# Optimization experiments

Hardware: AMD Instinct MI355X
Metric: run time of the kernel (lower is better)

The kernel has to match this reference:

```python
import jax, jax.numpy as jnp
import numpy as np

EPS = 1e-6     # vnn repo EPS used in VN nonlinearity / batchnorm norm
BN_EPS = 1e-5  # torch BatchNorm default eps
K = 40         # args.n_knn


def knn_idx(x, k):
    # x: (B, 3, N) -> (B, N, k) indices of k nearest neighbors (incl. self)
    inner = -2.0 * jnp.einsum('bdn,bdm->bnm', x, x)
    xx = jnp.sum(x * x, axis=1)  # (B, N)
    neg_dist = -xx[:, :, None] - inner - xx[:, None, :]
    _, idx = jax.lax.top_k(neg_dist, k)
    return idx


def get_graph_feature_cross(x, k):
    # x: (B, 3, N) -> (B, 3, 3, N, k): channels are [nbr - ctr, ctr, cross(nbr, ctr)]
    pts = jnp.transpose(x, (0, 2, 1))  # (B, N, 3)
    idx = knn_idx(x, k)                # (B, N, k)
    nbr = jax.vmap(lambda p, i: p[i])(pts, idx)          # (B, N, k, 3)
    ctr = jnp.broadcast_to(pts[:, :, None, :], nbr.shape)
    cross = jnp.cross(nbr, ctr)
    feat = jnp.stack([nbr - ctr, ctr, cross], axis=3)    # (B, N, k, 3, 3)
    return jnp.transpose(feat, (0, 3, 4, 1, 2))          # (B, C=3, 3vec, N, k)


def vn_bn(x):
    # VNBatchNorm (training-mode batch stats, affine = identity at init)
    # x: (B, C, 3, *rest); normalize the per-vector norm across (B, *rest)
    norm = jnp.sqrt(jnp.sum(x * x, axis=2)) + EPS  # (B, C, *rest)
    axes = (0,) + tuple(range(2, norm.ndim))
    mean = jnp.mean(norm, axis=axes, keepdims=True)
    var = jnp.var(norm, axis=axes, keepdims=True)
    norm_bn = (norm - mean) / jnp.sqrt(var + BN_EPS)
    return x / jnp.expand_dims(norm, 2) * jnp.expand_dims(norm_bn, 2)


def vn_lin(W, x):
    # channel-wise linear on axis 1 of (B, C, 3, ...)
    return jnp.einsum('oc,bc...->bo...', W, x)


def vn_lrelu(x, Wf, Wd):
    # VNLinearLeakyReLU with negative_slope=0.0
    p = vn_bn(vn_lin(Wf, x))
    d = vn_lin(Wd, x)
    dot = jnp.sum(p * d, axis=2, keepdims=True)
    dsq = jnp.sum(d * d, axis=2, keepdims=True)
    neg = p - (dot / (dsq + EPS)) * d  # project out the d component
    return jnp.where(dot >= 0, p, neg)


def vn_max_pool(x, W):
    # pool over last axis, picking the element maximizing <x, d> per (B, C, n)
    d = vn_lin(W, x)
    dot = jnp.sum(x * d, axis=2, keepdims=True)          # (B, C, 1, ..., K)
    idx = jnp.argmax(dot, axis=-1, keepdims=True)        # (B, C, 1, ..., 1)
    idx = jnp.broadcast_to(idx, x.shape[:-1] + (1,))
    return jnp.take_along_axis(x, idx, axis=-1)[..., 0]


def setup_inputs() -> dict:
    key = jax.random.key(0)
    ks = jax.random.split(key, 16)
    def w(k, o, i):
        bound = 1.0 / np.sqrt(i)  # torch nn.Linear default init
        return jax.random.uniform(k, (o, i), jnp.float32, -bound, bound)
    B, N = 8, 2048
    C1, C2, C3 = 64 // 3, 128 // 3, 1024 // 3  # 21, 42, 341
    F1, F2 = 512 // 3, 256 // 3                # 170, 85
    return {
        'x': jax.random.normal(ks[0], (B, 3, N), jnp.float32),
        'W_pos_feat': w(ks[1], C1, 3), 'W_pos_dir': w(ks[2], C1, 3),
        'W_gpool': w(ks[3], C1, C1),
        'W1_feat': w(ks[4], C1, C1), 'W1_dir': w(ks[5], C1, C1),
        'W2_feat': w(ks[6], C2, C1), 'W2_dir': w(ks[7], C2, C1),
        'W3_feat': w(ks[8], C3, C2), 'W3_dir': w(ks[9], C3, C2),
        'W_pool': w(ks[10], C3, C3),
        'Wf1_feat': w(ks[11], F1, C3), 'Wf1_dir': w(ks[12], F1, C3),
        'Wf2_feat': w(ks[13], F2, F1), 'Wf2_dir': w(ks[14], F2, F1),
        'Wf3': w(ks[15], 3, F2),
    }


def reference(x, W_pos_feat, W_pos_dir, W_gpool, W1_feat, W1_dir, W2_feat, W2_dir,
              W3_feat, W3_dir, W_pool, Wf1_feat, Wf1_dir, Wf2_feat, Wf2_dir, Wf3):
    feat = get_graph_feature_cross(x, K)            # (B, 3, 3, N, K)
    h = vn_lrelu(feat, W_pos_feat, W_pos_dir)       # (B, 21, 3, N, K)
    h = vn_max_pool(h, W_gpool)                     # (B, 21, 3, N)
    h = vn_lrelu(h, W1_feat, W1_dir)                # (B, 21, 3, N)
    h = vn_lrelu(h, W2_feat, W2_dir)                # (B, 42, 3, N)
    h = vn_lrelu(h, W3_feat, W3_dir)                # (B, 341, 3, N)
    h = vn_max_pool(h, W_pool)                      # (B, 341, 3)
    h = vn_lrelu(h, Wf1_feat, Wf1_dir)              # (B, 170, 3)
    h = vn_lrelu(h, Wf2_feat, Wf2_dir)              # (B, 85, 3)
    return vn_lin(Wf3, h)                           # (B, 3, 3)
```

## Files before the change

### kernel.cpp

```cpp
#include <hip/hip_runtime.h>

#define NP 2048
#define BATCH 8
#define KNN 40
#define EPSF 1e-6f
#define BNEPS 1e-5f

typedef __attribute__((ext_vector_type(8))) short short8;
typedef __attribute__((ext_vector_type(4))) float f32x4;

__device__ __forceinline__ unsigned ordf(float v){
  unsigned u = __float_as_uint(v);
  return (u & 0x80000000u) ? ~u : (u | 0x80000000u);
}

__device__ __forceinline__ void bsplit(float v, unsigned short &h, unsigned short &l){
  unsigned u = __float_as_uint(v);
  unsigned hu = (u + 0x7fffu + ((u >> 16) & 1u)) >> 16;
  h = (unsigned short)hu;
  float r = v - __uint_as_float(hu << 16);
  unsigned u2 = __float_as_uint(r);
  l = (unsigned short)((u2 + 0x7fffu + ((u2 >> 16) & 1u)) >> 16);
}

__device__ __forceinline__ float bf2f(unsigned short h){
  return __uint_as_float(((unsigned)h) << 16);
}

__global__ __launch_bounds__(256) void knn_kernel(const float* __restrict__ x, int* __restrict__ idx){
  __shared__ float4 sP[NP];
  int tid = threadIdx.x;
  int w = tid >> 6, lane = tid & 63;
  int row0 = blockIdx.x * 8 + w * 2, row1 = row0 + 1;
  int b = row0 >> 11;
  int i0 = row0 & 2047, i1 = row1 & 2047;
  const float* xb = x + b * 3 * NP;
  for (int t = tid; t < NP; t += 256){
    float a = xb[t], c = xb[NP + t], d = xb[2*NP + t];
    float xx = __fadd_rn(__fadd_rn(__fmul_rn(a,a), __fmul_rn(c,c)), __fmul_rn(d,d));
    sP[t] = make_float4(a, c, d, xx);
  }
  __syncthreads();
  float4 pa = sP[i0];
  float4 pb = sP[i1];
  const float4* lp = &sP[lane];
  unsigned long long a0 = 0, a1 = 0, a2 = 0, a3 = 0;
  unsigned long long b0 = 0, b1 = 0, b2 = 0, b3 = 0;
  #pragma unroll
  for (int m = 0; m < 32; m++){
    float4 pj = lp[m * 64];
    unsigned lowbits = (unsigned)(2047 - (m*64 + lane));
    float dotA = __fadd_rn(__fadd_rn(__fmul_rn(pa.x, pj.x), __fmul_rn(pa.y, pj.y)), __fmul_rn(pa.z, pj.z));
    float vA = __fsub_rn(__fsub_rn(-pa.w, __fmul_rn(-2.f, dotA)), pj.w);
    unsigned long long pkA = ((unsigned long long)ordf(vA) << 32) | lowbits;
    if (pkA > a3){
      if (pkA > a2){ a3 = a2; if (pkA > a1){ a2 = a1; if (pkA > a0){ a1 = a0; a0 = pkA; } else a1 = pkA; } else a2 = pkA; }
      else a3 = pkA;
    }
    float dotB = __fadd_rn(__fadd_rn(__fmul_rn(pb.x, pj.x), __fmul_rn(pb.y, pj.y)), __fmul_rn(pb.z, pj.z));
    float vB = __fsub_rn(__fsub_rn(-pb.w, __fmul_rn(-2.f, dotB)), pj.w);
    unsigned long long pkB = ((unsigned long long)ordf(vB) << 32) | lowbits;
    if (pkB > b3){
      if (pkB > b2){ b3 = b2; if (pkB > b1){ b2 = b1; if (pkB > b0){ b1 = b0; b0 = pkB; } else b1 = pkB; } else b2 = pkB; }
      else b3 = pkB;
    }
  }
  unsigned outA = 0, outB = 0;
  unsigned long long lastA = ~0ull, lastB = ~0ull;
  for (int kk = 0; kk < KNN; kk++){
    unsigned hvA = (unsigned)(a0 >> 32), hvB = (unsigned)(b0 >> 32);
    unsigned vmA = hvA, vmB = hvB;
    #pragma unroll
    for (int st = 32; st > 0; st >>= 1){
      unsigned oA = (unsigned)__shfl_xor((int)vmA, st, 64);
      unsigned oB = (unsigned)__shfl_xor((int)vmB, st, 64);
      vmA = (oA > vmA) ? oA : vmA;
      vmB = (oB > vmB) ? oB : vmB;
    }
    bool cA = (hvA == vmA), cB = (hvB == vmB);
    unsigned long long mA = __ballot(cA), mB = __ballot(cB);
    unsigned loA, loB;
    if (__popcll(mA) == 1){
      int wl = __ffsll((unsigned long long)mA) - 1;
      loA = (unsigned)__shfl((int)(unsigned)a0, wl, 64);
    } else {
      unsigned cl = cA ? (unsigned)a0 : 0u;
      #pragma unroll
      for (int st = 32; st > 0; st >>= 1){
        unsigned o = (unsigned)__shfl_xor((int)cl, st, 64);
        cl = (o > cl) ? o : cl;
      }
      loA = cl;
    }
    if (__popcll(mB) == 1){
      int wl = __ffsll((unsigned long long)mB) - 1;
      loB = (unsigned)__shfl((int)(unsigned)b0, wl, 64);
    } else {
      unsigned cl = cB ? (unsigned)b0 : 0u;
      #pragma unroll
      for (int st = 32; st > 0; st >>= 1){
        unsigned o = (unsigned)__shfl_xor((int)cl, st, 64);
        cl = (o > cl) ? o : cl;
      }
      loB = cl;
    }
    if (lane == kk){ outA = loA; outB = loB; }
    if (cA && (unsigned)a0 == loA){
      lastA = a0;
      a0 = a1; a1 = a2; a2 = a3; a3 = 0;
      if (a0 == 0){
        unsigned long long best = 0;
        #pragma unroll
        for (int m = 0; m < 32; m++){
          float4 pj = lp[m * 64];
          float dot = __fadd_rn(__fadd_rn(__fmul_rn(pa.x, pj.x), __fmul_rn(pa.y, pj.y)), __fmul_rn(pa.z, pj.z));
          float vv = __fsub_rn(__fsub_rn(-pa.w, __fmul_rn(-2.f, dot)), pj.w);
          unsigned long long pk = ((unsigned long long)ordf(vv) << 32) | (unsigned)(2047 - (m*64 + lane));
          if (pk < lastA && pk > best) best = pk;
        }
        a0 = best;
      }
    }
    if (cB && (unsigned)b0 == loB){
      lastB = b0;
      b0 = b1; b1 = b2; b2 = b3; b3 = 0;
      if (b0 == 0){
        unsigned long long best = 0;
        #pragma unroll
        for (int m = 0; m < 32; m++){
          float4 pj = lp[m * 64];
          float dot = __fadd_rn(__fadd_rn(__fmul_rn(pb.x, pj.x), __fmul_rn(pb.y, pj.y)), __fmul_rn(pb.z, pj.z));
          float vv = __fsub_rn(__fsub_rn(-pb.w, __fmul_rn(-2.f, dot)), pj.w);
          unsigned long long pk = ((unsigned long long)ordf(vv) << 32) | (unsigned)(2047 - (m*64 + lane));
          if (pk < lastB && pk > best) best = pk;
        }
        b0 = best;
      }
    }
  }
  if (lane < KNN){
    idx[row0 * KNN + lane] = 2047 - (int)outA;
    idx[row1 * KNN + lane] = 2047 - (int)outB;
  }
}

__global__ __launch_bounds__(256) void gf_stats(const float* __restrict__ x, const int* __restrict__ idx,
                                                const float* __restrict__ Wf, double* __restrict__ sums){
  int tid0 = blockIdx.x * 256 + threadIdx.x;
  float s[21], q[21];
  #pragma unroll
  for (int o = 0; o < 21; o++){ s[o] = 0.f; q[o] = 0.f; }
  for (int pix = tid0; pix < BATCH * NP * KNN; pix += 256 * 256){
    int rem = pix / KNN;
    int n = rem & 2047, b = rem >> 11;
    int j = idx[pix];
    const float* xb = x + b * 3 * NP;
    float c0 = xb[n], c1 = xb[NP + n], c2 = xb[2*NP + n];
    float a0 = xb[j], a1 = xb[NP + j], a2 = xb[2*NP + j];
    float r0 = a0 - c0, r1 = a1 - c1, r2 = a2 - c2;
    float g0 = a1*c2 - a2*c1, g1 = a2*c0 - a0*c2, g2 = a0*c1 - a1*c0;
    #pragma unroll
    for (int o = 0; o < 21; o++){
      float w0 = Wf[o*3], w1 = Wf[o*3+1], w2 = Wf[o*3+2];
      float p0 = w0*r0 + w1*c0 + w2*g0;
      float p1 = w0*r1 + w1*c1 + w2*g1;
      float p2 = w0*r2 + w1*c2 + w2*g2;
      float nm = sqrtf(p0*p0 + p1*p1 + p2*p2) + EPSF;
      s[o] += nm; q[o] += nm * nm;
    }
  }
  __shared__ float bs[4][42];
  int w = threadIdx.x >> 6;
  #pragma unroll
  for (int o = 0; o < 21; o++){
    float a = s[o], bb = q[o];
    #pragma unroll
    for (int st = 1; st < 64; st <<= 1){ a += __shfl_xor(a, st, 64); bb += __shfl_xor(bb, st, 64); }
    if ((threadIdx.x & 63) == 0){ bs[w][o] = a; bs[w][21 + o] = bb; }
  }
  __syncthreads();
  if (threadIdx.x < 42){
    float tot = bs[0][threadIdx.x] + bs[1][threadIdx.x] + bs[2][threadIdx.x] + bs[3][threadIdx.x];
    int o = threadIdx.x % 21, sq = threadIdx.x / 21;
    atomicAdd(&sums[2*o + sq], (double)tot);
  }
}

__global__ __launch_bounds__(320) void gf_applypool3(const float* __restrict__ x, const int* __restrict__ idx,
    const float* __restrict__ Wf, const float* __restrict__ Wd, const float* __restrict__ Wg,
    const float* __restrict__ mi, unsigned long long* __restrict__ packedGF){
  __shared__ unsigned long long sM[8*21];
  const int tid = threadIdx.x;
  for (int t = tid; t < 168; t += 320) sM[t] = 0ull;
  __syncthreads();
  const int pxl = tid / 40, k = tid - pxl * 40;
  const int px = blockIdx.x * 8 + pxl;
  const int b = px >> 11, n = px & 2047;
  const float* xb = x + b * 3 * NP;
  float c0 = xb[n], c1 = xb[NP + n], c2 = xb[2*NP + n];
  int j = idx[(size_t)px * KNN + k];
  float a0 = xb[j], a1 = xb[NP + j], a2 = xb[2*NP + j];
  float r0 = a0 - c0, r1 = a1 - c1, r2 = a2 - c2;
  float g0 = a1*c2 - a2*c1, g1 = a2*c0 - a0*c2, g2 = a0*c1 - a1*c0;
  float h[21][3];
  #pragma unroll
  for (int o = 0; o < 21; o++){
    float w0 = Wf[o*3], w1 = Wf[o*3+1], w2 = Wf[o*3+2];
    float p0 = w0*r0 + w1*c0 + w2*g0;
    float p1 = w0*r1 + w1*c1 + w2*g1;
    float p2 = w0*r2 + w1*c2 + w2*g2;
    float nm = sqrtf(p0*p0 + p1*p1 + p2*p2) + EPSF;
    float f = (nm - mi[2*o]) * mi[2*o+1] / nm;
    p0 *= f; p1 *= f; p2 *= f;
    float v0 = Wd[o*3], v1 = Wd[o*3+1], v2 = Wd[o*3+2];
    float d0 = v0*r0 + v1*c0 + v2*g0;
    float d1 = v0*r1 + v1*c1 + v2*g1;
    float d2 = v0*r2 + v1*c2 + v2*g2;
    float dot = p0*d0 + p1*d1 + p2*d2;
    float dsq = d0*d0 + d1*d1 + d2*d2;
    float t = dot / (dsq + EPSF);
    h[o][0] = (dot >= 0.f) ? p0 : fmaf(-t, d0, p0);
    h[o][1] = (dot >= 0.f) ? p1 : fmaf(-t, d1, p1);
    h[o][2] = (dot >= 0.f) ? p2 : fmaf(-t, d2, p2);
  }
  #pragma unroll
  for (int o = 0; o < 21; o++){
    float q0 = 0.f, q1 = 0.f, q2 = 0.f;
    #pragma unroll
    for (int c = 0; c < 21; c++){
      float wg = Wg[o*21 + c];
      q0 = fmaf(wg, h[c][0], q0); q1 = fmaf(wg, h[c][1], q1); q2 = fmaf(wg, h[c][2], q2);
    }
    float dp = q0*h[o][0] + q1*h[o][1] + q2*h[o][2];
    unsigned long long pk = ((unsigned long long)ordf(dp) << 32) | (unsigned)(63 - k);
    atomicMax(&sM[pxl*21 + o], pk);
  }
  __syncthreads();
  for (int t = tid; t < 168; t += 320){
    int lpx = t / 21, lo = t - lpx * 21;
    packedGF[(size_t)(blockIdx.x * 8 + lpx) * 21 + lo] = sM[t];
  }
}

__global__ __launch_bounds__(256) void gf_gather(const float* __restrict__ x, const int* __restrict__ idx,
    const float* __restrict__ Wf, const float* __restrict__ Wd, const float* __restrict__ mi,
    const unsigned long long* __restrict__ packedGF, float* __restrict__ h1){
  int t = blockIdx.x * 256 + threadIdx.x;
  if (t >= BATCH * NP * 21) return;
  int px = t / 21, o = t - px * 21;
  int b = px >> 11, n = px & 2047;
  int k = 63 - (int)(packedGF[t] & 0xffffffffu);
  int j = idx[(size_t)px * KNN + k];
  const float* xb = x + b * 3 * NP;
  float c0 = xb[n], c1 = xb[NP + n], c2 = xb[2*NP + n];
  float a0 = xb[j], a1 = xb[NP + j], a2 = xb[2*NP + j];
  float r0 = a0 - c0, r1 = a1 - c1, r2 = a2 - c2;
  float g0 = a1*c2 - a2*c1, g1 = a2*c0 - a0*c2, g2 = a0*c1 - a1*c0;
  float w0 = Wf[o*3], w1 = Wf[o*3+1], w2 = Wf[o*3+2];
  float p0 = w0*r0 + w1*c0 + w2*g0;
  float p1 = w0*r1 + w1*c1 + w2*g1;
  float p2 = w0*r2 + w1*c2 + w2*g2;
  float nm = sqrtf(p0*p0 + p1*p1 + p2*p2) + EPSF;
  float f = (nm - mi[2*o]) * mi[2*o+1] / nm;
  p0 *= f; p1 *= f; p2 *= f;
  float v0 = Wd[o*3], v1 = Wd[o*3+1], v2 = Wd[o*3+2];
  float d0 = v0*r0 + v1*c0 + v2*g0;
  float d1 = v0*r1 + v1*c1 + v2*g1;
  float d2 = v0*r2 + v1*c2 + v2*g2;
  float dot = p0*d0 + p1*d1 + p2*d2;
  float dsq = d0*d0 + d1*d1 + d2*d2;
  float tt = dot / (dsq + EPSF);
  float o0 = (dot >= 0.f) ? p0 : fmaf(-tt, d0, p0);
  float o1 = (dot >= 0.f) ? p1 : fmaf(-tt, d1, p1);
  float o2 = (dot >= 0.f) ? p2 : fmaf(-tt, d2, p2);
  float* dst = h1 + (size_t)((b*21 + o)*3) * NP + n;
  dst[0] = o0; dst[NP] = o1; dst[2*NP] = o2;
}

template<int CIN>
__global__ __launch_bounds__(256) void layer_stats2(const float* __restrict__ hin, const float* __restrict__ Wf,
                                                    double* __restrict__ sums, int Co){
  const int px0 = blockIdx.x * 1024;
  const int b = px0 >> 11;
  const int n0 = (px0 & 2047) + (threadIdx.x << 2);
  const int o0 = blockIdx.y * 8;
  const float* hb = hin + (size_t)b * CIN * 3 * NP + n0;
  float p[8][3][4];
  #pragma unroll
  for (int oo = 0; oo < 8; oo++)
    #pragma unroll
    for (int e = 0; e < 3; e++)
      #pragma unroll
      for (int k = 0; k < 4; k++) p[oo][e][k] = 0.f;
  for (int c = 0; c < CIN; c++){
    float4 hv[3];
    #pragma unroll
    for (int e = 0; e < 3; e++) hv[e] = *(const float4*)&hb[(size_t)(c*3 + e) * NP];
    #pragma unroll
    for (int oo = 0; oo < 8; oo++){
      int o = o0 + oo; if (o >= Co) o = Co - 1;
      float wv = Wf[o*CIN + c];
      #pragma unroll
      for (int e = 0; e < 3; e++){
        p[oo][e][0] = fmaf(wv, hv[e].x, p[oo][e][0]);
        p[oo][e][1] = fmaf(wv, hv[e].y, p[oo][e][1]);
        p[oo][e][2] = fmaf(wv, hv[e].z, p[oo][e][2]);
        p[oo][e][3] = fmaf(wv, hv[e].w, p[oo][e][3]);
      }
    }
  }
  float sl[8], ql[8];
  #pragma unroll
  for (int oo = 0; oo < 8; oo++){
    sl[oo] = 0.f; ql[oo] = 0.f;
    #pragma unroll
    for (int k = 0; k < 4; k++){
      float nm = sqrtf(p[oo][0][k]*p[oo][0][k] + p[oo][1][k]*p[oo][1][k] + p[oo][2][k]*p[oo][2][k]) + EPSF;
      sl[oo] += nm; ql[oo] += nm * nm;
    }
  }
  __shared__ float red[4][16];
  int w = threadIdx.x >> 6;
  #pragma unroll
  for (int oo = 0; oo < 8; oo++){
    float sv = sl[oo], qv = ql[oo];
    #pragma unroll
    for (int st = 1; st < 64; st <<= 1){ sv += __shfl_xor(sv, st, 64); qv += __shfl_xor(qv, st, 64); }
    if ((threadIdx.x & 63) == 0){ red[w][oo] = sv; red[w][8 + oo] = qv; }
  }
  __syncthreads();
  if (threadIdx.x < 16){
    float tot = red[0][threadIdx.x] + red[1][threadIdx.x] + red[2][threadIdx.x] + red[3][threadIdx.x];
    int oo = threadIdx.x & 7, isq = threadIdx.x >> 3;
    int o = o0 + oo;
    if (o < Co) atomicAdd(&sums[2*o + isq], (double)tot);
  }
}

template<int CIN>
__global__ __launch_bounds__(256) void layer_apply2(const float* __restrict__ hin, const float* __restrict__ Wf,
    const float* __restrict__ Wd, const float* __restrict__ mi, float* __restrict__ hout, int Co){
  const int px = blockIdx.x * 256 + threadIdx.x;
  const int b = px >> 11, n = px & 2047;
  const int o0 = blockIdx.y * 8;
  const float* hb = hin + (size_t)b * CIN * 3 * NP + n;
  float p[8][3], d[8][3];
  #pragma unroll
  for (int oo = 0; oo < 8; oo++)
    #pragma unroll
    for (int e = 0; e < 3; e++){ p[oo][e] = 0.f; d[oo][e] = 0.f; }
  for (int c = 0; c < CIN; c++){
    float h0 = hb[(size_t)(c*3 + 0) * NP];
    float h1 = hb[(size_t)(c*3 + 1) * NP];
    float h2 = hb[(size_t)(c*3 + 2) * NP];
    #pragma unroll
    for (int oo = 0; oo < 8; oo++){
      int o = o0 + oo; if (o >= Co) o = Co - 1;
      float wf = Wf[o*CIN + c], wd = Wd[o*CIN + c];
      p[oo][0] = fmaf(wf, h0, p[oo][0]); p[oo][1] = fmaf(wf, h1, p[oo][1]); p[oo][2] = fmaf(wf, h2, p[oo][2]);
      d[oo][0] = fmaf(wd, h0, d[oo][0]); d[oo][1] = fmaf(wd, h1, d[oo][1]); d[oo][2] = fmaf(wd, h2, d[oo][2]);
    }
  }
  #pragma unroll
  for (int oo = 0; oo < 8; oo++){
    int o = o0 + oo;
    if (o < Co){
      float nm = sqrtf(p[oo][0]*p[oo][0] + p[oo][1]*p[oo][1] + p[oo][2]*p[oo][2]) + EPSF;
      float f = (nm - mi[2*o]) * mi[2*o+1] / nm;
      float p0 = p[oo][0]*f, p1 = p[oo][1]*f, p2 = p[oo][2]*f;
      float dot = p0*d[oo][0] + p1*d[oo][1] + p2*d[oo][2];
      float dsq = d[oo][0]*d[oo][0] + d[oo][1]*d[oo][1] + d[oo][2]*d[oo][2];
      float t = dot / (dsq + EPSF);
      float r0 = (dot >= 0.f) ? p0 : fmaf(-t, d[oo][0], p0);
      float r1 = (dot >= 0.f) ? p1 : fmaf(-t, d[oo][1], p1);
      float r2 = (dot >= 0.f) ? p2 : fmaf(-t, d[oo][2], p2);
      float* dst = hout + (size_t)((b*Co + o)*3) * NP + n;
      dst[0] = r0; dst[NP] = r1; dst[2*NP] = r2;
    }
  }
}

__global__ __launch_bounds__(256) void layer_apply_l3v2(const float* __restrict__ hin, const float* __restrict__ Wf,
    const float* __restrict__ Wd, const float* __restrict__ mi,
    unsigned short* __restrict__ Hkh, unsigned short* __restrict__ Hkl){
  const int px = blockIdx.x * 256 + threadIdx.x;
  const int b = px >> 11, n = px & 2047;
  const int o0 = blockIdx.y * 8;
  const float* hb = hin + (size_t)b * 42 * 3 * NP + n;
  float r[8][3];
  #pragma unroll
  for (int oo = 0; oo < 8; oo++)
    #pragma unroll
    for (int e = 0; e < 3; e++) r[oo][e] = 0.f;
  if (o0 < 341){
    float p[8][3], d[8][3];
    #pragma unroll
    for (int oo = 0; oo < 8; oo++)
      #pragma unroll
      for (int e = 0; e < 3; e++){ p[oo][e] = 0.f; d[oo][e] = 0.f; }
    for (int c = 0; c < 42; c++){
      float h0 = hb[(size_t)(c*3 + 0) * NP];
      float h1 = hb[(size_t)(c*3 + 1) * NP];
      float h2 = hb[(size_t)(c*3 + 2) * NP];
      #pragma unroll
      for (int oo = 0; oo < 8; oo++){
        int o = o0 + oo; if (o >= 341) o = 340;
        float wf = Wf[o*42 + c], wd = Wd[o*42 + c];
        p[oo][0] = fmaf(wf, h0, p[oo][0]); p[oo][1] = fmaf(wf, h1, p[oo][1]); p[oo][2] = fmaf(wf, h2, p[oo][2]);
        d[oo][0] = fmaf(wd, h0, d[oo][0]); d[oo][1] = fmaf(wd, h1, d[oo][1]); d[oo][2] = fmaf(wd, h2, d[oo][2]);
      }
    }
    #pragma unroll
    for (int oo = 0; oo < 8; oo++){
      int o = o0 + oo;
      if (o < 341){
        float nm = sqrtf(p[oo][0]*p[oo][0] + p[oo][1]*p[oo][1] + p[oo][2]*p[oo][2]) + EPSF;
        float f = (nm - mi[2*o]) * mi[2*o+1] / nm;
        float p0 = p[oo][0]*f, p1 = p[oo][1]*f, p2 = p[oo][2]*f;
        float dot = p0*d[oo][0] + p1*d[oo][1] + p2*d[oo][2];
        float dsq = d[oo][0]*d[oo][0] + d[oo][1]*d[oo][1] + d[oo][2]*d[oo][2];
        float t = dot / (dsq + EPSF);
        r[oo][0] = (dot >= 0.f) ? p0 : fmaf(-t, d[oo][0], p0);
        r[oo][1] = (dot >= 0.f) ? p1 : fmaf(-t, d[oo][1], p1);
        r[oo][2] = (dot >= 0.f) ? p2 : fmaf(-t, d[oo][2], p2);
      }
    }
  }
  #pragma unroll
  for (int e = 0; e < 3; e++){
    unsigned ph[4], pl[4];
    #pragma unroll
    for (int oo = 0; oo < 8; oo++){
      unsigned short hh, ll;
      bsplit(r[oo][e], hh, ll);
      if (!(oo & 1)){ ph[oo>>1] = hh; pl[oo>>1] = ll; }
      else { ph[oo>>1] |= ((unsigned)hh) << 16; pl[oo>>1] |= ((unsigned)ll) << 16; }
    }
    size_t base = ((((size_t)(b*3 + e))*48 + blockIdx.y) * 2048 + n) * 8;
    *(uint4*)(Hkh + base) = make_uint4(ph[0], ph[1], ph[2], ph[3]);
    *(uint4*)(Hkl + base) = make_uint4(pl[0], pl[1], pl[2], pl[3]);
  }
}

__global__ void finalize_stats(const double* __restrict__ sums, float* __restrict__ mi, int Co, double invM){
  int o = blockIdx.x * 64 + threadIdx.x;
  if (o >= Co) return;
  double m = sums[2*o] * invM;
  double v = sums[2*o+1] * invM - m * m;
  if (v < 0.0) v = 0.0;
  mi[2*o] = (float)m;
  mi[2*o+1] = (float)(1.0 / sqrt(v + (double)BNEPS));
}

__global__ __launch_bounds__(256) void wk_kernel(const float* __restrict__ Wp,
    unsigned short* __restrict__ Wkh, unsigned short* __restrict__ Wkl){
  int t = blockIdx.x * 256 + threadIdx.x;
  if (t >= 44*384*8) return;
  int j = t & 7, o = (t >> 3) % 384, cb = t / (384*8);
  int c = cb*8 + j;
  float v = (c < 341 && o < 341) ? Wp[o*341 + c] : 0.f;
  unsigned short h, l;
  bsplit(v, h, l);
  Wkh[t] = h; Wkl[t] = l;
}

__global__ __launch_bounds__(256) void pool_mfma(const unsigned short* __restrict__ Wkh,
    const unsigned short* __restrict__ Wkl, const unsigned short* __restrict__ Hkh,
    const unsigned short* __restrict__ Hkl, unsigned long long* __restrict__ packed){
  __shared__ unsigned short sB[2][2][4][64][8];
  const int b = blockIdx.z, o0 = blockIdx.y * 128, n0 = blockIdx.x * 64;
  const int t = threadIdx.x, w = t >> 6, l = t & 63;
  const int wo = o0 + w * 32;
  const int r = l & 15, g = l >> 4;
  const int skb = t >> 6, sn = t & 63;
  const int ktw = wo >> 5;

  f32x4 acc[2][4], dotv[2][4], hval[2][4];
  #pragma unroll
  for (int s = 0; s < 2; s++)
    #pragma unroll
    for (int nt = 0; nt < 4; nt++){ dotv[s][nt] = (f32x4)0.f; hval[s][nt] = (f32x4)0.f; }

  auto gsrc = [&](const unsigned short* base, int e, int kt) -> const uint4* {
    return (const uint4*)(base + ((((size_t)(b*3 + e))*48 + (size_t)(kt*4 + skb)) * 2048 + n0 + sn) * 8);
  };

  uint4 rg[2];
  rg[0] = *gsrc(Hkh, 0, 0);
  rg[1] = *gsrc(Hkl, 0, 0);

  for (int ek = 0; ek < 33; ek++){
    const int e = ek / 11, kt = ek - e*11, buf = ek & 1;
    *(uint4*)&sB[buf][0][skb][sn][0] = rg[0];
    *(uint4*)&sB[buf][1][skb][sn][0] = rg[1];
    __syncthreads();
    if (ek < 32){
      int e2 = (ek+1) / 11, kt2 = (ek+1) - e2*11;
      rg[0] = *gsrc(Hkh, e2, kt2);
      rg[1] = *gsrc(Hkl, e2, kt2);
    }
    if (kt == 0){
      #pragma unroll
      for (int s = 0; s < 2; s++)
        #pragma unroll
        for (int nt = 0; nt < 4; nt++) acc[s][nt] = (f32x4)0.f;
    }
    short8 ah[2], al[2];
    #pragma unroll
    for (int s = 0; s < 2; s++){
      size_t aoff = (((size_t)(kt*4 + g)) * 384 + (wo + s*16 + r)) * 8;
      ah[s] = *(const short8*)(Wkh + aoff);
      al[s] = *(const short8*)(Wkl + aoff);
    }
    #pragma unroll
    for (int nt = 0; nt < 4; nt++){
      short8 bh = *(const short8*)&sB[buf][0][g][nt*16 + r][0];
      short8 bl = *(const short8*)&sB[buf][1][g][nt*16 + r][0];
      #pragma unroll
      for (int s = 0; s < 2; s++){
        acc[s][nt] = __builtin_amdgcn_mfma_f32_16x16x32_bf16(ah[s], bh, acc[s][nt], 0, 0, 0);
        acc[s][nt] = __builtin_amdgcn_mfma_f32_16x16x32_bf16(ah[s], bl, acc[s][nt], 0, 0, 0);
        acc[s][nt] = __builtin_amdgcn_mfma_f32_16x16x32_bf16(al[s], bh, acc[s][nt], 0, 0, 0);
      }
    }
    if (kt == ktw){
      #pragma unroll
      for (int s = 0; s < 2; s++){
        #pragma unroll
        for (int jj = 0; jj < 4; jj++){
          int oin = s*16 + g*4 + jj;
          #pragma unroll
          for (int nt = 0; nt < 4; nt++){
            hval[s][nt][jj] = bf2f(sB[buf][0][oin>>3][nt*16 + r][oin&7])
                            + bf2f(sB[buf][1][oin>>3][nt*16 + r][oin&7]);
          }
        }
      }
    }
    __syncthreads();
    if (kt == 10){
      #pragma unroll
      for (int s = 0; s < 2; s++)
        #pragma unroll
        for (int nt = 0; nt < 4; nt++)
          #pragma unroll
          for (int jj = 0; jj < 4; jj++)
            dotv[s][nt][jj] += acc[s][nt][jj] * hval[s][nt][jj];
    }
  }
  #pragma unroll
  for (int s = 0; s < 2; s++){
    #pragma unroll
    for (int j = 0; j < 4; j++){
      int o = wo + s*16 + g*4 + j;
      unsigned long long best = 0;
      #pragma unroll
      for (int nt = 0; nt < 4; nt++){
        int n = n0 + nt*16 + r;
        unsigned long long pk = ((unsigned long long)ordf(dotv[s][nt][j]) << 32) | (unsigned)(2047 - n);
        if (pk > best) best = pk;
      }
      #pragma unroll
      for (int st = 1; st < 16; st <<= 1){
        unsigned long long ob = __shfl_xor(best, st, 64);
        if (ob > best) best = ob;
      }
      if (r == 0 && o < 341) atomicMax(&packed[b*341 + o], best);
    }
  }
}

__global__ void pool_gather(const unsigned long long* __restrict__ packed,
                            const unsigned short* __restrict__ Hkh, const unsigned short* __restrict__ Hkl,
                            float* __restrict__ pooled){
  int t = blockIdx.x * 256 + threadIdx.x;
  if (t >= BATCH * 341) return;
  int n = 2047 - (int)(packed[t] & 0xffffffffu);
  int b = t / 341, o = t % 341;
  #pragma unroll
  for (int e = 0; e < 3; e++){
    size_t hb = ((((size_t)(b*3 + e))*48 + (o >> 3)) * 2048 + n) * 8 + (o & 7);
    pooled[t*3 + e] = bf2f(Hkh[hb]) + bf2f(Hkl[hb]);
  }
}

__global__ __launch_bounds__(64) void flayer(const float* __restrict__ in, const float* __restrict__ Wf,
    const float* __restrict__ Wd, float* __restrict__ out, int Cin, int Co){
  int o = blockIdx.x, lane = threadIdx.x;
  float pv[24], dv[24];
  #pragma unroll
  for (int be = 0; be < 24; be++){ pv[be] = 0.f; dv[be] = 0.f; }
  for (int c = lane; c < Cin; c += 64){
    float wf = Wf[o*Cin + c], wd = Wd[o*Cin + c];
    #pragma unroll
    for (int bb = 0; bb < 8; bb++){
      #pragma unroll
      for (int e = 0; e < 3; e++){
        float hv = in[(bb*Cin + c)*3 + e];
        pv[bb*3+e] = fmaf(wf, hv, pv[bb*3+e]);
        dv[bb*3+e] = fmaf(wd, hv, dv[bb*3+e]);
      }
    }
  }
  #pragma unroll
  for (int be = 0; be < 24; be++){
    #pragma unroll
    for (int st = 1; st < 64; st <<= 1){
      pv[be] += __shfl_xor(pv[be], st, 64);
      dv[be] += __shfl_xor(dv[be], st, 64);
    }
  }
  float nm[8], dotb[8], dsqb[8];
  float mean = 0.f;
  #pragma unroll
  for (int bb = 0; bb < 8; bb++){
    nm[bb] = sqrtf(pv[bb*3]*pv[bb*3] + pv[bb*3+1]*pv[bb*3+1] + pv[bb*3+2]*pv[bb*3+2]) + EPSF;
    mean += nm[bb];
  }
  mean *= 0.125f;
  float var = 0.f;
  #pragma unroll
  for (int bb = 0; bb < 8; bb++){ float dvv = nm[bb] - mean; var += dvv * dvv; }
  var *= 0.125f;
  float istd = 1.f / sqrtf(var + BNEPS);
  #pragma unroll
  for (int bb = 0; bb < 8; bb++){
    float f = (nm[bb] - mean) * istd / nm[bb];
    dotb[bb] = f * (pv[bb*3]*dv[bb*3] + pv[bb*3+1]*dv[bb*3+1] + pv[bb*3+2]*dv[bb*3+2]);
    dsqb[bb] = dv[bb*3]*dv[bb*3] + dv[bb*3+1]*dv[bb*3+1] + dv[bb*3+2]*dv[bb*3+2];
  }
  #pragma unroll
  for (int be = 0; be < 24; be++){
    if (lane == be){
      int bb = be / 3;
      float f = (nm[bb] - mean) * istd / nm[bb];
      float pe = pv[be] * f;
      float t = dotb[bb] / (dsqb[bb] + EPSF);
      float res = (dotb[bb] >= 0.f) ? pe : fmaf(-t, dv[be], pe);
      out[(bb*Co + o)*3 + (be % 3)] = res;
    }
  }
}

__global__ void final_lin(const float* __restrict__ in, const float* __restrict__ W, float* __restrict__ out){
  int t = threadIdx.x;
  if (t >= 72) return;
  int b = t / 9, o = (t % 9) / 3, e = t % 3;
  float s = 0.f;
  for (int c = 0; c < 85; c++) s = fmaf(W[o*85 + c], in[(b*85 + c)*3 + e], s);
  out[t] = s;
}

extern "C" void kernel_launch(void* const* d_in, const int* in_sizes, int n_in,
                              void* d_out, int out_size, void* d_ws, size_t ws_size,
                              hipStream_t stream){
  const float* x   = (const float*)d_in[0];
  const float* Wpf = (const float*)d_in[1];
  const float* Wpd = (const float*)d_in[2];
  const float* Wg  = (const float*)d_in[3];
  const float* W1f = (const float*)d_in[4];
  const float* W1d = (const float*)d_in[5];
  const float* W2f = (const float*)d_in[6];
  const float* W2d = (const float*)d_in[7];
  const float* W3f = (const float*)d_in[8];
  const float* W3d = (const float*)d_in[9];
  const float* Wpool = (const float*)d_in[10];
  const float* Wf1f = (const float*)d_in[11];
  const float* Wf1d = (const float*)d_in[12];
  const float* Wf2f = (const float*)d_in[13];
  const float* Wf2d = (const float*)d_in[14];
  const float* Wf3  = (const float*)d_in[15];
  float* out = (float*)d_out;

  char* ws = (char*)d_ws;
  size_t off = 0;
  int*   idx  = (int*)(ws + off);             off += (size_t)BATCH*NP*KNN*4;
  unsigned long long* packedGF = (unsigned long long*)(ws + off); off += (size_t)BATCH*NP*21*8;
  float* h1  = (float*)(ws + off);            off += (size_t)BATCH*21*3*NP*4;
  float* h2  = (float*)(ws + off);            off += (size_t)BATCH*21*3*NP*4;
  float* h3  = (float*)(ws + off);            off += (size_t)BATCH*42*3*NP*4;
  unsigned short* Hkh = (unsigned short*)(ws + off); off += (size_t)BATCH*3*48*NP*8*2;
  unsigned short* Hkl = (unsigned short*)(ws + off); off += (size_t)BATCH*3*48*NP*8*2;
  unsigned short* Wkh = (unsigned short*)(ws + off); off += (size_t)44*384*8*2;
  unsigned short* Wkl = (unsigned short*)(ws + off); off += (size_t)44*384*8*2;
  char*  zbase = ws + off;
  double* sums_gf = (double*)(ws + off);      off += 8192;
  double* sums_l1 = (double*)(ws + off);      off += 8192;
  double* sums_l2 = (double*)(ws + off);      off += 8192;
  double* sums_l3 = (double*)(ws + off);      off += 8192;
  unsigned long long* packed = (unsigned long long*)(ws + off); off += 24576;
  size_t zbytes = (ws + off) - zbase;
  float* mi_gf = (float*)(ws + off);          off += 1024;
  float* mi_l1 = (float*)(ws + off);          off += 1024;
  float* mi_l2 = (float*)(ws + off);          off += 1024;
  float* mi_l3 = (float*)(ws + off);          off += 4096;
  float* pooled = (float*)(ws + off);         off += (size_t)BATCH*341*3*4 + 32;
  float* h5 = (float*)(ws + off);             off += (size_t)BATCH*170*3*4 + 32;
  float* h6 = (float*)(ws + off);             off += (size_t)BATCH*85*3*4 + 32;

  hipMemsetAsync(zbase, 0, zbytes, stream);

  knn_kernel<<<BATCH*NP/8, 256, 0, stream>>>(x, idx);
  wk_kernel<<<(44*384*8 + 255)/256, 256, 0, stream>>>(Wpool, Wkh, Wkl);

  gf_stats<<<256, 256, 0, stream>>>(x, idx, Wpf, sums_gf);
  finalize_stats<<<1, 64, 0, stream>>>(sums_gf, mi_gf, 21, 1.0 / (double)(BATCH*NP*KNN));
  gf_applypool3<<<BATCH*NP/8, 320, 0, stream>>>(x, idx, Wpf, Wpd, Wg, mi_gf, packedGF);
  gf_gather<<<(BATCH*NP*21 + 255)/256, 256, 0, stream>>>(x, idx, Wpf, Wpd, mi_gf, packedGF, h1);

  layer_stats2<21><<<dim3(16,3), 256, 0, stream>>>(h1, W1f, sums_l1, 21);
  finalize_stats<<<1, 64, 0, stream>>>(sums_l1, mi_l1, 21, 1.0 / (double)(BATCH*NP));
  layer_apply2<21><<<dim3(64,3), 256, 0, stream>>>(h1, W1f, W1d, mi_l1, h2, 21);

  layer_stats2<21><<<dim3(16,6), 256, 0, stream>>>(h2, W2f, sums_l2, 42);
  finalize_stats<<<1, 64, 0, stream>>>(sums_l2, mi_l2, 42, 1.0 / (double)(BATCH*NP));
  layer_apply2<21><<<dim3(64,6), 256, 0, stream>>>(h2, W2f, W2d, mi_l2, h3, 42);

  layer_stats2<42><<<dim3(16,43), 256, 0, stream>>>(h3, W3f, sums_l3, 341);
  finalize_stats<<<6, 64, 0, stream>>>(sums_l3, mi_l3, 341, 1.0 / (double)(BATCH*NP));
  layer_apply_l3v2<<<dim3(64,44), 256, 0, stream>>>(h3, W3f, W3d, mi_l3, Hkh, Hkl);

  pool_mfma<<<dim3(32, 3, BATCH), 256, 0, stream>>>(Wkh, Wkl, Hkh, Hkl, packed);
  pool_gather<<<(BATCH*341 + 255)/256, 256, 0, stream>>>(packed, Hkh, Hkl, pooled);

  flayer<<<170, 64, 0, stream>>>(pooled, Wf1f, Wf1d, h5, 341, 170);
  flayer<<<85, 64, 0, stream>>>(h5, Wf2f, Wf2d, h6, 170, 85);
  final_lin<<<1, 128, 0, stream>>>(h6, Wf3, out);
}
```

Measured before the change: 490.9 us.

## Move layer-3 VN linear stats and apply onto split-bf16 MFMA

Layer 2 now writes its output directly as hi/lo bf16-split blocks of 8 channels instead of fp32. The layer-3 statistics and apply passes then run as MFMA GEMMs (three-term bf16 split to keep near-fp32 accuracy) over 64x64 output tiles, replacing scalar FMA loops over 42 input channels for 341 outputs. This targets the FMA-bound layer-3 work and removes a separate fp32 intermediate, in exchange for extra weight-preparation kernels, atomics and split-precision rounding error.

```diff
diff --git a/kernel.cpp b/kernel.cpp
--- a/kernel.cpp
+++ b/kernel.cpp
@@ -380,40 +380,40 @@
   }
 }
 
-__global__ __launch_bounds__(256) void layer_apply_l3v2(const float* __restrict__ hin, const float* __restrict__ Wf,
+__global__ __launch_bounds__(256) void layer_apply2_k(const float* __restrict__ hin, const float* __restrict__ Wf,
     const float* __restrict__ Wd, const float* __restrict__ mi,
-    unsigned short* __restrict__ Hkh, unsigned short* __restrict__ Hkl){
+    unsigned short* __restrict__ Hk3h, unsigned short* __restrict__ Hk3l){
   const int px = blockIdx.x * 256 + threadIdx.x;
   const int b = px >> 11, n = px & 2047;
-  const int o0 = blockIdx.y * 8;
-  const float* hb = hin + (size_t)b * 42 * 3 * NP + n;
+  const int kb = blockIdx.y;
+  const float* hb = hin + (size_t)b * 21 * 3 * NP + n;
   float r[8][3];
   #pragma unroll
   for (int oo = 0; oo < 8; oo++)
     #pragma unroll
     for (int e = 0; e < 3; e++) r[oo][e] = 0.f;
-  if (o0 < 341){
+  if (kb < 6){
     float p[8][3], d[8][3];
     #pragma unroll
     for (int oo = 0; oo < 8; oo++)
       #pragma unroll
       for (int e = 0; e < 3; e++){ p[oo][e] = 0.f; d[oo][e] = 0.f; }
-    for (int c = 0; c < 42; c++){
+    for (int c = 0; c < 21; c++){
       float h0 = hb[(size_t)(c*3 + 0) * NP];
       float h1 = hb[(size_t)(c*3 + 1) * NP];
       float h2 = hb[(size_t)(c*3 + 2) * NP];
       #pragma unroll
       for (int oo = 0; oo < 8; oo++){
-        int o = o0 + oo; if (o >= 341) o = 340;
-        float wf = Wf[o*42 + c], wd = Wd[o*42 + c];
+        int o = kb*8 + oo; if (o >= 42) o = 41;
+        float wf = Wf[o*21 + c], wd = Wd[o*21 + c];
         p[oo][0] = fmaf(wf, h0, p[oo][0]); p[oo][1] = fmaf(wf, h1, p[oo][1]); p[oo][2] = fmaf(wf, h2, p[oo][2]);
         d[oo][0] = fmaf(wd, h0, d[oo][0]); d[oo][1] = fmaf(wd, h1, d[oo][1]); d[oo][2] = fmaf(wd, h2, d[oo][2]);
       }
     }
     #pragma unroll
     for (int oo = 0; oo < 8; oo++){
-      int o = o0 + oo;
-      if (o < 341){
+      int o = kb*8 + oo;
+      if (o < 42){
         float nm = sqrtf(p[oo][0]*p[oo][0] + p[oo][1]*p[oo][1] + p[oo][2]*p[oo][2]) + EPSF;
         float f = (nm - mi[2*o]) * mi[2*o+1] / nm;
         float p0 = p[oo][0]*f, p1 = p[oo][1]*f, p2 = p[oo][2]*f;
@@ -436,9 +436,9 @@
       if (!(oo & 1)){ ph[oo>>1] = hh; pl[oo>>1] = ll; }
       else { ph[oo>>1] |= ((unsigned)hh) << 16; pl[oo>>1] |= ((unsigned)ll) << 16; }
     }
-    size_t base = ((((size_t)(b*3 + e))*48 + blockIdx.y) * 2048 + n) * 8;
-    *(uint4*)(Hkh + base) = make_uint4(ph[0], ph[1], ph[2], ph[3]);
-    *(uint4*)(Hkl + base) = make_uint4(pl[0], pl[1], pl[2], pl[3]);
+    size_t base = ((((size_t)(b*3 + e))*8 + kb) * 2048 + n) * 8;
+    *(uint4*)(Hk3h + base) = make_uint4(ph[0], ph[1], ph[2], ph[3]);
+    *(uint4*)(Hk3l + base) = make_uint4(pl[0], pl[1], pl[2], pl[3]);
   }
 }
 
@@ -462,6 +462,165 @@
   unsigned short h, l;
   bsplit(v, h, l);
   Wkh[t] = h; Wkl[t] = l;
+}
+
+__global__ __launch_bounds__(256) void wk3_kernel(const float* __restrict__ W3f, const float* __restrict__ W3d,
+    unsigned short* __restrict__ Wfh, unsigned short* __restrict__ Wfl,
+    unsigned short* __restrict__ Wdh, unsigned short* __restrict__ Wdl){
+  int t = blockIdx.x * 256 + threadIdx.x;
+  if (t >= 8*384*8) return;
+  int j = t & 7, o = (t >> 3) % 384, cb = t / (384*8);
+  int c = cb*8 + j;
+  bool ok = (c < 42 && o < 341);
+  float vf = ok ? W3f[o*42 + c] : 0.f;
+  float vd = ok ? W3d[o*42 + c] : 0.f;
+  unsigned short h, l;
+  bsplit(vf, h, l); Wfh[t] = h; Wfl[t] = l;
+  bsplit(vd, h, l); Wdh[t] = h; Wdl[t] = l;
+}
+
+__global__ __launch_bounds__(256) void stats3_mfma(const unsigned short* __restrict__ Wfh,
+    const unsigned short* __restrict__ Wfl, const unsigned short* __restrict__ Hh,
+    const unsigned short* __restrict__ Hl, double* __restrict__ sums){
+  __shared__ unsigned short sB[2][8][64][8];
+  const int b = blockIdx.z, o0 = blockIdx.y * 64, n0 = blockIdx.x * 64;
+  const int t = threadIdx.x, w = t >> 6, l = t & 63;
+  const int r = l & 15, g = l >> 4;
+  const int wo = o0 + w * 16;
+  const int skb = t >> 5, sn = (t & 31) * 2;
+  f32x4 acc[3][4];
+  #pragma unroll
+  for (int e = 0; e < 3; e++)
+    #pragma unroll
+    for (int nt = 0; nt < 4; nt++) acc[e][nt] = (f32x4)0.f;
+  for (int e = 0; e < 3; e++){
+    if (e) __syncthreads();
+    const uint4* srcH = (const uint4*)(Hh + ((((size_t)(b*3 + e))*8 + skb) * 2048 + n0 + sn) * 8);
+    const uint4* srcL = (const uint4*)(Hl + ((((size_t)(b*3 + e))*8 + skb) * 2048 + n0 + sn) * 8);
+    uint4 h0 = srcH[0], h1 = srcH[1], l0 = srcL[0], l1 = srcL[1];
+    *(uint4*)&sB[0][skb][sn][0] = h0; *(uint4*)&sB[0][skb][sn+1][0] = h1;
+    *(uint4*)&sB[1][skb][sn][0] = l0; *(uint4*)&sB[1][skb][sn+1][0] = l1;
+    __syncthreads();
+    #pragma unroll
+    for (int kt = 0; kt < 2; kt++){
+      size_t aoff = (((size_t)(kt*4 + g)) * 384 + wo + r) * 8;
+      short8 ah = *(const short8*)(Wfh + aoff);
+      short8 al = *(const short8*)(Wfl + aoff);
+      #pragma unroll
+      for (int nt = 0; nt < 4; nt++){
+        short8 bh = *(const short8*)&sB[0][kt*4 + g][nt*16 + r][0];
+        short8 bl = *(const short8*)&sB[1][kt*4 + g][nt*16 + r][0];
+        acc[e][nt] = __builtin_amdgcn_mfma_f32_16x16x32_bf16(ah, bh, acc[e][nt], 0, 0, 0);
+        acc[e][nt] = __builtin_amdgcn_mfma_f32_16x16x32_bf16(ah, bl, acc[e][nt], 0, 0, 0);
+        acc[e][nt] = __builtin_amdgcn_mfma_f32_16x16x32_bf16(al, bh, acc[e][nt], 0, 0, 0);
+      }
+    }
+  }
+  #pragma unroll
+  for (int jj = 0; jj < 4; jj++){
+    int o = wo + g*4 + jj;
+    float s1 = 0.f, s2 = 0.f;
+    #pragma unroll
+    for (int nt = 0; nt < 4; nt++){
+      float p0 = acc[0][nt][jj], p1 = acc[1][nt][jj], p2 = acc[2][nt][jj];
+      float nm = sqrtf(p0*p0 + p1*p1 + p2*p2) + EPSF;
+      s1 += nm; s2 += nm * nm;
+    }
+    #pragma unroll
+    for (int st = 1; st < 16; st <<= 1){
+      s1 += __shfl_xor(s1, st, 64);
+      s2 += __shfl_xor(s2, st, 64);
+    }
+    if (r == 0 && o < 341){
+      atomicAdd(&sums[2*o], (double)s1);
+      atomicAdd(&sums[2*o+1], (double)s2);
+    }
+  }
+}
+
+__global__ __launch_bounds__(256) void apply3_mfma(const unsigned short* __restrict__ Wfh,
+    const unsigned short* __restrict__ Wfl, const unsigned short* __restrict__ Wdh,
+    const unsigned short* __restrict__ Wdl, const unsigned short* __restrict__ Hh,
+    const unsigned short* __restrict__ Hl, const float* __restrict__ mi,
+    unsigned short* __restrict__ Hkh, unsigned short* __restrict__ Hkl){
+  __shared__ unsigned short sB[2][8][64][8];
+  const int b = blockIdx.z, o0 = blockIdx.y * 64, n0 = blockIdx.x * 64;
+  const int t = threadIdx.x, w = t >> 6, l = t & 63;
+  const int r = l & 15, g = l >> 4;
+  const int wo = o0 + w * 16;
+  const int skb = t >> 5, sn = (t & 31) * 2;
+  f32x4 accp[3][4], accd[3][4];
+  #pragma unroll
+  for (int e = 0; e < 3; e++)
+    #pragma unroll
+    for (int nt = 0; nt < 4; nt++){ accp[e][nt] = (f32x4)0.f; accd[e][nt] = (f32x4)0.f; }
+  for (int e = 0; e < 3; e++){
+    if (e) __syncthreads();
+    const uint4* srcH = (const uint4*)(Hh + ((((size_t)(b*3 + e))*8 + skb) * 2048 + n0 + sn) * 8);
+    const uint4* srcL = (const uint4*)(Hl + ((((size_t)(b*3 + e))*8 + skb) * 2048 + n0 + sn) * 8);
+    uint4 h0 = srcH[0], h1 = srcH[1], l0 = srcL[0], l1 = srcL[1];
+    *(uint4*)&sB[0][skb][sn][0] = h0; *(uint4*)&sB[0][skb][sn+1][0] = h1;
+    *(uint4*)&sB[1][skb][sn][0] = l0; *(uint4*)&sB[1][skb][sn+1][0] = l1;
+    __syncthreads();
+    #pragma unroll
+    for (int kt = 0; kt < 2; kt++){
+      size_t aoff = (((size_t)(kt*4 + g)) * 384 + wo + r) * 8;
+      short8 afh = *(const short8*)(Wfh + aoff);
+      short8 afl = *(const short8*)(Wfl + aoff);
+      short8 adh = *(const short8*)(Wdh + aoff);
+      short8 adl = *(const short8*)(Wdl + aoff);
+      #pragma unroll
+      for (int nt = 0; nt < 4; nt++){
+        short8 bh = *(const short8*)&sB[0][kt*4 + g][nt*16 + r][0];
+        short8 bl = *(const short8*)&sB[1][kt*4 + g][nt*16 + r][0];
+        accp[e][nt] = __builtin_amdgcn_mfma_f32_16x16x32_bf16(afh, bh, accp[e][nt], 0, 0, 0);
+        accp[e][nt] = __builtin_amdgcn_mfma_f32_16x16x32_bf16(afh, bl, accp[e][nt], 0, 0, 0);
+        accp[e][nt] = __builtin_amdgcn_mfma_f32_16x16x32_bf16(afl, bh, accp[e][nt], 0, 0, 0);
+        accd[e][nt] = __builtin_amdgcn_mfma_f32_16x16x32_bf16(adh, bh, accd[e][nt], 0, 0, 0);
+        accd[e][nt] = __builtin_amdgcn_mfma_f32_16x16x32_bf16(adh, bl, accd[e][nt], 0, 0, 0);
+        accd[e][nt] = __builtin_amdgcn_mfma_f32_16x16x32_bf16(adl, bh, accd[e][nt], 0, 0, 0);
+      }
+    }
+  }
+  const int obase = wo + g*4;
+  const int kb = obase >> 3, jo = obase & 7;
+  #pragma unroll
+  for (int nt = 0; nt < 4; nt++){
+    float rr[3][4];
+    #pragma unroll
+    for (int jj = 0; jj < 4; jj++){
+      int o = obase + jj;
+      float r0 = 0.f, r1 = 0.f, r2 = 0.f;
+      if (o < 341){
+        float p0 = accp[0][nt][jj], p1 = accp[1][nt][jj], p2 = accp[2][nt][jj];
+        float d0 = accd[0][nt][jj], d1 = accd[1][nt][jj], d2 = accd[2][nt][jj];
+        float nm = sqrtf(p0*p0 + p1*p1 + p2*p2) + EPSF;
+        float f = (nm - mi[2*o]) * mi[2*o+1] / nm;
+        p0 *= f; p1 *= f; p2 *= f;
+        float dot = p0*d0 + p1*d1 + p2*d2;
+        float dsq = d0*d0 + d1*d1 + d2*d2;
+        float tt = dot / (dsq + EPSF);
+        r0 = (dot >= 0.f) ? p0 : fmaf(-tt, d0, p0);
+        r1 = (dot >= 0.f) ? p1 : fmaf(-tt, d1, p1);
+        r2 = (dot >= 0.f) ? p2 : fmaf(-tt, d2, p2);
+      }
+      rr[0][jj] = r0; rr[1][jj] = r1; rr[2][jj] = r2;
+    }
+    int n = n0 + nt*16 + r;
+    #pragma unroll
+    for (int e = 0; e < 3; e++){
+      unsigned short h0, l0, h1, l1, h2, l2, h3, l3;
+      bsplit(rr[e][0], h0, l0); bsplit(rr[e][1], h1, l1);
+      bsplit(rr[e][2], h2, l2); bsplit(rr[e][3], h3, l3);
+      unsigned ph0 = (unsigned)h0 | ((unsigned)h1 << 16);
+      unsigned ph1 = (unsigned)h2 | ((unsigned)h3 << 16);
+      unsigned pl0 = (unsigned)l0 | ((unsigned)l1 << 16);
+      unsigned pl1 = (unsigned)l2 | ((unsigned)l3 << 16);
+      size_t base = ((((size_t)(b*3 + e))*48 + kb) * 2048 + (size_t)n) * 8 + jo;
+      *(uint2*)(Hkh + base) = make_uint2(ph0, ph1);
+      *(uint2*)(Hkl + base) = make_uint2(pl0, pl1);
+    }
+  }
 }
 
 __global__ __launch_bounds__(256) void pool_mfma(const unsigned short* __restrict__ Wkh,
@@ -678,11 +837,16 @@
   unsigned long long* packedGF = (unsigned long long*)(ws + off); off += (size_t)BATCH*NP*21*8;
   float* h1  = (float*)(ws + off);            off += (size_t)BATCH*21*3*NP*4;
   float* h2  = (float*)(ws + off);            off += (size_t)BATCH*21*3*NP*4;
-  float* h3  = (float*)(ws + off);            off += (size_t)BATCH*42*3*NP*4;
+  unsigned short* Hk3h = (unsigned short*)(ws + off); off += (size_t)BATCH*3*8*NP*8*2;
+  unsigned short* Hk3l = (unsigned short*)(ws + off); off += (size_t)BATCH*3*8*NP*8*2;
   unsigned short* Hkh = (unsigned short*)(ws + off); off += (size_t)BATCH*3*48*NP*8*2;
   unsigned short* Hkl = (unsigned short*)(ws + off); off += (size_t)BATCH*3*48*NP*8*2;
   unsigned short* Wkh = (unsigned short*)(ws + off); off += (size_t)44*384*8*2;
   unsigned short* Wkl = (unsigned short*)(ws + off); off += (size_t)44*384*8*2;
+  unsigned short* Wk3fh = (unsigned short*)(ws + off); off += (size_t)8*384*8*2;
+  unsigned short* Wk3fl = (unsigned short*)(ws + off); off += (size_t)8*384*8*2;
+  unsigned short* Wk3dh = (unsigned short*)(ws + off); off += (size_t)8*384*8*2;
+  unsigned short* Wk3dl = (unsigned short*)(ws + off); off += (size_t)8*384*8*2;
   char*  zbase = ws + off;
   double* sums_gf = (double*)(ws + off);      off += 8192;
   double* sums_l1 = (double*)(ws + off);      off += 8192;
@@ -702,6 +866,7 @@
 
   knn_kernel<<<BATCH*NP/8, 256, 0, stream>>>(x, idx);
   wk_kernel<<<(44*384*8 + 255)/256, 256, 0, stream>>>(Wpool, Wkh, Wkl);
+  wk3_kernel<<<(8*384*8 + 255)/256, 256, 0, stream>>>(W3f, W3d, Wk3fh, Wk3fl, Wk3dh, Wk3dl);
 
   gf_stats<<<256, 256, 0, stream>>>(x, idx, Wpf, sums_gf);
   finalize_stats<<<1, 64, 0, stream>>>(sums_gf, mi_gf, 21, 1.0 / (double)(BATCH*NP*KNN));
@@ -714,11 +879,11 @@
 
   layer_stats2<21><<<dim3(16,6), 256, 0, stream>>>(h2, W2f, sums_l2, 42);
   finalize_stats<<<1, 64, 0, stream>>>(sums_l2, mi_l2, 42, 1.0 / (double)(BATCH*NP));
-  layer_apply2<21><<<dim3(64,6), 256, 0, stream>>>(h2, W2f, W2d, mi_l2, h3, 42);
-
-  layer_stats2<42><<<dim3(16,43), 256, 0, stream>>>(h3, W3f, sums_l3, 341);
+  layer_apply2_k<<<dim3(64,8), 256, 0, stream>>>(h2, W2f, W2d, mi_l2, Hk3h, Hk3l);
+
+  stats3_mfma<<<dim3(32, 6, BATCH), 256, 0, stream>>>(Wk3fh, Wk3fl, Hk3h, Hk3l, sums_l3);
   finalize_stats<<<6, 64, 0, stream>>>(sums_l3, mi_l3, 341, 1.0 / (double)(BATCH*NP));
-  layer_apply_l3v2<<<dim3(64,44), 256, 0, stream>>>(h3, W3f, W3d, mi_l3, Hkh, Hkl);
+  apply3_mfma<<<dim3(32, 6, BATCH), 256, 0, stream>>>(Wk3fh, Wk3fl, Wk3dh, Wk3dl, Hk3h, Hk3l, mi_l3, Hkh, Hkl);
 
   pool_mfma<<<dim3(32, 3, BATCH), 256, 0, stream>>>(Wkh, Wkl, Hkh, Hkl, packed);
   pool_gather<<<(BATCH*341 + 255)/256, 256, 0, stream>>>(packed, Hkh, Hkl, pooled);
```

Result: faster. 469.9 us (-4.3%).
